# Optimization experiments

Measured on AMD Instinct MI355X. Metric: run time of the kernel, lower is better.

The kernel has to match this reference:

```python
import jax, jax.numpy as jnp
import numpy as np

N_DRUG = 572
EMB = 512
K_NB = 64
SEG_NB = 16
BN_EPS = 1e-5


def setup_inputs() -> dict:
    key = jax.random.key(0)
    ks = jax.random.split(key, 8)
    return {
        "drug_name": jnp.arange(N_DRUG, dtype=jnp.int64) if jax.config.jax_enable_x64 else jnp.arange(N_DRUG, dtype=jnp.int32),
        "adj_tail": jax.random.randint(ks[0], (N_DRUG, K_NB), 0, 100000),
        "adj_relation": jax.random.randint(ks[1], (N_DRUG, K_NB), 0, 200),
        "inv_adj_idx": jax.random.randint(ks[2], (N_DRUG, SEG_NB), 0, N_DRUG),
        "drug_table": jax.random.normal(ks[3], (N_DRUG, EMB), dtype=jnp.float32),
        "rela_table": jax.random.normal(ks[4], (200, EMB), dtype=jnp.float32),
        "ent_table": jax.random.normal(ks[5], (100000, EMB), dtype=jnp.float32),
        "W_lin": jax.random.normal(ks[6], (2 * EMB, EMB), dtype=jnp.float32) * (1.0 / np.sqrt(2 * EMB)),
        "b_lin": jnp.zeros((EMB,), jnp.float32),
        "bn_gamma": jnp.ones((EMB,), jnp.float32),
        "bn_beta": jnp.zeros((EMB,), jnp.float32),
        "epoch": 2,
    }


def _forward(drug_name, adj_tail, adj_relation, inv_adj_idx,
             drug_table, rela_table, ent_table, W_lin, b_lin,
             bn_gamma, bn_beta, epoch):
    # Embedding gathers
    drug_emb = drug_table[drug_name]          # [N, D]
    rel_emb = rela_table[adj_relation]        # [N, K, D]
    ent_emb = ent_table[adj_tail]             # [N, K, D]

    # KGCN-style attention over sampled neighbors: score_k = softmax(drug . rel_k)
    scores = jax.nn.softmax(jnp.einsum('nd,nkd->nk', drug_emb, rel_emb), axis=1)
    attended = jnp.einsum('nk,nkd->nd', scores, ent_emb)  # [N, D]

    # Linear -> ReLU -> BatchNorm1d (training-mode batch stats, biased var)
    e = jnp.concatenate([attended, drug_emb], axis=1)     # [N, 2D]
    h = jax.nn.relu(e @ W_lin + b_lin)                    # [N, D]
    mu = jnp.mean(h, axis=0)
    var = jnp.mean(jnp.square(h - mu), axis=0)
    drug_f = bn_gamma * (h - mu) * jax.lax.rsqrt(var + BN_EPS) + bn_beta

    if epoch > 1:
        # Sequential in-place neighbor averaging (faithful to the Python loop:
        # later drugs see already-updated rows).
        def body(f, x):
            i, pos = x
            avg = jnp.mean(f[pos], axis=0)                # [D]
            f = f.at[i].set((avg + f[i]) * 0.5)
            return f, None
        idxs = jnp.arange(N_DRUG)
        drug_f, _ = jax.lax.scan(body, drug_f, (idxs, inv_adj_idx))
    return drug_f


def reference(drug_name, adj_tail, adj_relation, inv_adj_idx,
              drug_table, rela_table, ent_table, W_lin, b_lin,
              bn_gamma, bn_beta, epoch):
    return _forward(drug_name, adj_tail, adj_relation, inv_adj_idx,
                    drug_table, rela_table, ent_table, W_lin, b_lin,
                    bn_gamma, bn_beta, epoch)
```

## Files before the change

### kernel.cpp

```cpp
#include <hip/hip_runtime.h>
#include <hip/hip_bf16.h>

#define N_DRUG 572
#define EMB    512
#define K_NB   64
#define SEG_NB 16
#define SCOLS  16

typedef __hip_bfloat16  bf16;
typedef __hip_bfloat162 bf162;

__device__ __forceinline__ float b2f(bf16 x){ return __bfloat162float(x); }
__device__ __forceinline__ float bflo(unsigned u){ return __uint_as_float(u << 16); }
__device__ __forceinline__ float bfhi(unsigned u){ return __uint_as_float(u & 0xffff0000u); }
__device__ __forceinline__ unsigned pack_bf2(float a, float b) {
    bf162 v; v.x = __float2bfloat16(a); v.y = __float2bfloat16(b);
    unsigned u; __builtin_memcpy(&u, &v, 4); return u;
}

template<typename T> __device__ __forceinline__ float ldf(const T* p);
template<> __device__ __forceinline__ float ldf<float>(const float* p){ return *p; }
template<> __device__ __forceinline__ float ldf<bf16>(const bf16* p){ return b2f(*p); }

template<typename T> __device__ __forceinline__ float2 ld2(const T* p);
template<> __device__ __forceinline__ float2 ld2<float>(const float* p){ return *(const float2*)p; }
template<> __device__ __forceinline__ float2 ld2<bf16>(const bf16* p){
    bf162 v = *(const bf162*)p; return make_float2(b2f(v.x), b2f(v.y));
}

template<typename T> __device__ __forceinline__ void st2(T* p, float x, float y);
template<> __device__ __forceinline__ void st2<float>(float* p, float x, float y){ *(float2*)p = make_float2(x, y); }
template<> __device__ __forceinline__ void st2<bf16>(bf16* p, float x, float y){
    bf162 v; v.x = __float2bfloat16(x); v.y = __float2bfloat16(y); *(bf162*)p = v;
}

struct F8 { float v[8]; };
template<typename T> __device__ __forceinline__ F8 ld8(const T* p);
template<> __device__ __forceinline__ F8 ld8<float>(const float* p){
    F8 r; const float4 a = ((const float4*)p)[0], b = ((const float4*)p)[1];
    r.v[0]=a.x; r.v[1]=a.y; r.v[2]=a.z; r.v[3]=a.w;
    r.v[4]=b.x; r.v[5]=b.y; r.v[6]=b.z; r.v[7]=b.w; return r;
}
template<> __device__ __forceinline__ F8 ld8<bf16>(const bf16* p){
    F8 r; const uint4 u = *(const uint4*)p;
    r.v[0]=bflo(u.x); r.v[1]=bfhi(u.x); r.v[2]=bflo(u.y); r.v[3]=bfhi(u.y);
    r.v[4]=bflo(u.z); r.v[5]=bfhi(u.z); r.v[6]=bflo(u.w); r.v[7]=bfhi(u.w);
    return r;
}

__device__ __forceinline__ bool idx_is64(const void* drug_name) {
    return ((const int*)drug_name)[1] == 0;
}
__device__ __forceinline__ int ld_idx(const void* p, int i, bool is64) {
    return is64 ? (int)((const long long*)p)[i] : ((const int*)p)[i];
}

__device__ __forceinline__ bool detect_bf16(const void* tab) {
    const int lane = threadIdx.x & 63;
    int hit = 0;
    if (lane < 32) {
        const unsigned u = ((const unsigned*)tab)[lane * 997];
        const unsigned e = (u >> 7) & 0xffu;
        hit = (e >= 110u && e <= 141u) ? 1 : 0;
    }
    return __popcll(__ballot(hit)) >= 24;
}

struct __align__(16) FwdSmem {
    float e[2 * EMB];
    float part[4][EMB];
    float sc[K_NB];
    int   tl[K_NB];
    int   rl[K_NB];
};

template<typename T>
__device__ void fwd_impl(FwdSmem& sm,
    const void* drug_name, const void* adj_tail, const void* adj_rel,
    const T* __restrict__ drug_table, const T* __restrict__ rela_table,
    const T* __restrict__ ent_table,  const T* __restrict__ W,
    const T* __restrict__ bl, T* __restrict__ h)
{
    const int  t    = threadIdx.x;
    const int  wave = t >> 6, lane = t & 63;
    const int  n    = blockIdx.x;
    const bool is64 = idx_is64(drug_name);

    {
        const int row = ld_idx(drug_name, n, is64);
        const float2 v = ld2(drug_table + (size_t)row * EMB + 2 * t);
        sm.e[EMB + 2 * t]     = v.x;
        sm.e[EMB + 2 * t + 1] = v.y;
        if (t < K_NB) {
            sm.tl[t] = ld_idx(adj_tail, n * K_NB + t, is64);
            sm.rl[t] = ld_idx(adj_rel,  n * K_NB + t, is64);
        }
    }
    __syncthreads();

    F8 ed;
    {
        const float4 e0 = ((const float4*)&sm.e[EMB + 8 * lane])[0];
        const float4 e1 = ((const float4*)&sm.e[EMB + 8 * lane])[1];
        ed.v[0]=e0.x; ed.v[1]=e0.y; ed.v[2]=e0.z; ed.v[3]=e0.w;
        ed.v[4]=e1.x; ed.v[5]=e1.y; ed.v[6]=e1.z; ed.v[7]=e1.w;
    }

    {
        #pragma unroll 4
        for (int kk = 0; kk < 16; ++kk) {
            const int k = 16 * wave + kk;
            const F8 rv = ld8(rela_table + (size_t)sm.rl[k] * EMB + 8 * lane);
            float p = 0.f;
            #pragma unroll
            for (int m = 0; m < 8; ++m) p = fmaf(ed.v[m], rv.v[m], p);
            #pragma unroll
            for (int off = 32; off; off >>= 1) p += __shfl_xor(p, off, 64);
            if (lane == 0) sm.sc[k] = p;
        }
    }
    __syncthreads();

    if (t < 64) {
        const float s = sm.sc[t];
        float m = s;
        #pragma unroll
        for (int off = 32; off; off >>= 1) m = fmaxf(m, __shfl_xor(m, off, 64));
        const float ex = __expf(s - m);
        float sum = ex;
        #pragma unroll
        for (int off = 32; off; off >>= 1) sum += __shfl_xor(sum, off, 64);
        sm.sc[t] = ex / sum;
    }
    __syncthreads();

    {
        float a[8];
        #pragma unroll
        for (int m = 0; m < 8; ++m) a[m] = 0.f;
        #pragma unroll 4
        for (int kk = 0; kk < 16; ++kk) {
            const int k = 16 * wave + kk;
            const float wgt = sm.sc[k];
            const F8 v = ld8(ent_table + (size_t)sm.tl[k] * EMB + 8 * lane);
            #pragma unroll
            for (int m = 0; m < 8; ++m) a[m] = fmaf(wgt, v.v[m], a[m]);
        }
        float4* pp = (float4*)&sm.part[wave][8 * lane];
        pp[0] = make_float4(a[0], a[1], a[2], a[3]);
        pp[1] = make_float4(a[4], a[5], a[6], a[7]);
    }
    __syncthreads();

    {
        float2 s = make_float2(0.f, 0.f);
        #pragma unroll
        for (int w = 0; w < 4; ++w) {
            const float2 pw = *(const float2*)&sm.part[w][2 * t];
            s.x += pw.x; s.y += pw.y;
        }
        sm.e[2 * t]     = s.x;
        sm.e[2 * t + 1] = s.y;
    }
    __syncthreads();

    {
        float acc[8];
        #pragma unroll
        for (int m = 0; m < 8; ++m) acc[m] = 0.f;
        const int j0 = wave * 256;
        #pragma unroll 4
        for (int j = 0; j < 256; ++j) {
            const float ej = sm.e[j0 + j];
            const F8 w8 = ld8(W + (size_t)(j0 + j) * EMB + 8 * lane);
            #pragma unroll
            for (int m = 0; m < 8; ++m) acc[m] = fmaf(ej, w8.v[m], acc[m]);
        }
        float4* pp = (float4*)&sm.part[wave][8 * lane];
        pp[0] = make_float4(acc[0], acc[1], acc[2], acc[3]);
        pp[1] = make_float4(acc[4], acc[5], acc[6], acc[7]);
    }
    __syncthreads();

    {
        const int d0 = 2 * t;
        const float2 bb = ld2(bl + d0);
        float x = bb.x, y = bb.y;
        #pragma unroll
        for (int w = 0; w < 4; ++w) {
            const float2 pw = *(const float2*)&sm.part[w][d0];
            x += pw.x; y += pw.y;
        }
        st2(h + (size_t)n * EMB + d0, fmaxf(x, 0.f), fmaxf(y, 0.f));
    }
}

__global__ __launch_bounds__(256) void k_fwd(
    const void* drug_name, const void* adj_tail, const void* adj_rel,
    const void* drug_tab, const void* rela_tab, const void* ent_tab,
    const void* W, const void* bl, void* h)
{
    __shared__ FwdSmem sm;
    if (detect_bf16(drug_tab))
        fwd_impl<bf16>(sm, drug_name, adj_tail, adj_rel,
                       (const bf16*)drug_tab, (const bf16*)rela_tab,
                       (const bf16*)ent_tab, (const bf16*)W,
                       (const bf16*)bl, (bf16*)h);
    else
        fwd_impl<float>(sm, drug_name, adj_tail, adj_rel,
                        (const float*)drug_tab, (const float*)rela_tab,
                        (const float*)ent_tab, (const float*)W,
                        (const float*)bl, (float*)h);
}

struct __align__(16) ScanSmem {
    float    fbuf[N_DRUG * SCOLS];
    unsigned obuf[N_DRUG * SEG_NB];
    float4   corr[576];
};

template<typename T>
__device__ __forceinline__ void stage_fbuf(float* fbuf, const T* h, int c0, int t);
template<>
__device__ __forceinline__ void stage_fbuf<float>(float* fbuf, const float* h, int c0, int t) {
    float4* dst = (float4*)fbuf;
    #pragma unroll 4
    for (int k = t; k < N_DRUG * 4; k += 64)
        dst[k] = *(const float4*)(h + (size_t)(k >> 2) * EMB + c0 + 4 * (k & 3));
}
template<>
__device__ __forceinline__ void stage_fbuf<bf16>(float* fbuf, const bf16* h, int c0, int t) {
    float4* dst = (float4*)fbuf;
    #pragma unroll 4
    for (int k = t; k < N_DRUG * 2; k += 64) {
        const uint4 v = *(const uint4*)(h + (size_t)(k >> 1) * EMB + c0 + 8 * (k & 1));
        dst[2 * k]     = make_float4(bflo(v.x), bfhi(v.x), bflo(v.y), bfhi(v.y));
        dst[2 * k + 1] = make_float4(bflo(v.z), bfhi(v.z), bflo(v.w), bfhi(v.w));
    }
}

template<typename T>
__device__ __forceinline__ void flush_fbuf(const float* fbuf, T* h, int c0, int t);
template<>
__device__ __forceinline__ void flush_fbuf<float>(const float* fbuf, float* h, int c0, int t) {
    const float4* src = (const float4*)fbuf;
    #pragma unroll 4
    for (int k = t; k < N_DRUG * 4; k += 64)
        *(float4*)(h + (size_t)(k >> 2) * EMB + c0 + 4 * (k & 3)) = src[k];
}
template<>
__device__ __forceinline__ void flush_fbuf<bf16>(const float* fbuf, bf16* h, int c0, int t) {
    const float4* src = (const float4*)fbuf;
    #pragma unroll 4
    for (int k = t; k < N_DRUG * 2; k += 64) {
        const float4 f0 = src[2 * k], f1 = src[2 * k + 1];
        uint4 o;
        o.x = pack_bf2(f0.x, f0.y); o.y = pack_bf2(f0.z, f0.w);
        o.z = pack_bf2(f1.x, f1.y); o.w = pack_bf2(f1.z, f1.w);
        *(uint4*)(h + (size_t)(k >> 1) * EMB + c0 + 8 * (k & 1)) = o;
    }
}

template<bool IS64>
__device__ __forceinline__ void stage_obuf(unsigned* obuf, const void* inv, int t) {
    const uint4* src = (const uint4*)inv;
    if (IS64) {
        #pragma unroll 4
        for (int k = t; k < (N_DRUG * SEG_NB) / 2; k += 64) {
            const uint4 v = src[k];
            *(uint2*)(obuf + 2 * k) = make_uint2(v.x << 4, v.z << 4);
        }
    } else {
        uint4* dst = (uint4*)obuf;
        #pragma unroll 4
        for (int k = t; k < (N_DRUG * SEG_NB) / 4; k += 64) {
            uint4 v = src[k];
            v.x <<= 4; v.y <<= 4; v.z <<= 4; v.w <<= 4;
            dst[k] = v;
        }
    }
}

#define RMIN(X) (((X) < N_DRUG) ? (X) : (N_DRUG - 1))

#define BODY4(Vg, Qg, Sc, Fc, Cc, Vr, Sr, I)                                 \
    {                                                                        \
        Vg.x = fb[Qg.x + c]; Vg.y = fb[Qg.y + c];                            \
        Vg.z = fb[Qg.z + c]; Vg.w = fb[Qg.w + c];                            \
        Qg = ob4[RMIN((I) + 7) * 4 + g];                                     \
        float nv = fmaf(Sc, 1.f / 32.f, Fc * 0.5f);                          \
        nv = fmaf(Cc.x, nv1 - f1, nv);                                       \
        nv = fmaf(Cc.y, nv2 - f2, nv);                                       \
        nv = fmaf(Cc.z, nv3 - f3, nv);                                       \
        f3 = f2; f2 = f1; f1 = Fc; nv3 = nv2; nv2 = nv1; nv1 = nv;           \
        if (g == 0) sm.fbuf[(I) * SCOLS + c] = nv;                           \
        Fc = fb[RMIN((I) + 4) * 16 + c];                                     \
        Cc = sm.corr[(I) + 4];                                               \
        float l = (Vr.x + Vr.y) + (Vr.z + Vr.w);                             \
        Sr = (l + __shfl_xor(l, 16, 64)) +                                   \
             (__shfl_xor(l, 32, 64) + __shfl_xor(l, 48, 64));                \
    }

template<typename T, bool IS64>
__device__ void scan_impl(ScanSmem& sm, T* __restrict__ h,
    const void* __restrict__ inv, const T* __restrict__ gamma,
    const T* __restrict__ beta, const void* __restrict__ epoch)
{
    const int t  = threadIdx.x;
    const int c0 = blockIdx.x * SCOLS;

    stage_obuf<IS64>(sm.obuf, inv, t);
    stage_fbuf<T>(sm.fbuf, h, c0, t);
    for (int k = t; k < 576; k += 64) sm.corr[k] = make_float4(0.f, 0.f, 0.f, 0.f);
    __syncthreads();

    for (int i = 1 + t; i < N_DRUG; i += 64) {
        const unsigned tA = (unsigned)(i - 1) << 4;
        const unsigned tB = (unsigned)(i - 2) << 4;
        const unsigned tC = (unsigned)(i - 3) << 4;
        int cA = 0, cB = 0, cC = 0;
        #pragma unroll
        for (int j = 0; j < SEG_NB; ++j) {
            const unsigned o = sm.obuf[i * SEG_NB + j];
            cA += (o == tA) ? 1 : 0;
            cB += (o == tB) ? 1 : 0;
            cC += (o == tC) ? 1 : 0;
        }
        sm.corr[i] = make_float4((float)cA * (1.f / 32.f),
                                 (float)cB * (1.f / 32.f),
                                 (float)cC * (1.f / 32.f), 0.f);
    }

    {
        const int c = t & 15, g = t >> 4;
        float s = 0.f, s2 = 0.f;
        for (int r = g; r < N_DRUG; r += 4) {
            const float x = sm.fbuf[r * SCOLS + c];
            s += x; s2 = fmaf(x, x, s2);
        }
        s  += __shfl_xor(s, 16, 64);  s  += __shfl_xor(s, 32, 64);
        s2 += __shfl_xor(s2, 16, 64); s2 += __shfl_xor(s2, 32, 64);
        const float mu  = s * (1.f / N_DRUG);
        const float var = fmaxf(s2 * (1.f / N_DRUG) - mu * mu, 0.f);
        const float gs  = ldf(gamma + c0 + c) * rsqrtf(var + 1e-5f);
        const float bs  = ldf(beta  + c0 + c);
        for (int r = g; r < N_DRUG; r += 4) {
            const float x = sm.fbuf[r * SCOLS + c];
            sm.fbuf[r * SCOLS + c] = fmaf(x - mu, gs, bs);
        }
    }
    __syncthreads();

    if (((const int*)epoch)[0] > 1) {
        const int c = t & 15, g = t >> 4;
        const float* fb  = sm.fbuf;
        const uint4* ob4 = (const uint4*)sm.obuf;

        float4 V0, V1, V2, V3;
        uint4  Q0, Q1, Q2, Q3;

        {
            const uint4 o0 = ob4[0 * 4 + g], o1 = ob4[1 * 4 + g], o2 = ob4[2 * 4 + g];
            V0.x = fb[o0.x + c]; V0.y = fb[o0.y + c];
            V0.z = fb[o0.z + c]; V0.w = fb[o0.w + c];
            V1.x = fb[o1.x + c]; V1.y = fb[o1.y + c];
            V1.z = fb[o1.z + c]; V1.w = fb[o1.w + c];
            V2.x = fb[o2.x + c]; V2.y = fb[o2.y + c];
            V2.z = fb[o2.z + c]; V2.w = fb[o2.w + c];
        }
        Q3 = ob4[3 * 4 + g];
        Q0 = ob4[4 * 4 + g]; Q1 = ob4[5 * 4 + g]; Q2 = ob4[6 * 4 + g];
        float F0 = fb[0 * 16 + c], F1 = fb[1 * 16 + c];
        float F2 = fb[2 * 16 + c], F3 = fb[3 * 16 + c];
        float4 C0 = sm.corr[0], C1 = sm.corr[1];
        float4 C2 = sm.corr[2], C3 = sm.corr[3];
        float S0, S1, S2 = 0.f, S3 = 0.f;
        {
            float l0 = (V0.x + V0.y) + (V0.z + V0.w);
            S0 = (l0 + __shfl_xor(l0, 16, 64)) +
                 (__shfl_xor(l0, 32, 64) + __shfl_xor(l0, 48, 64));
            float l1 = (V1.x + V1.y) + (V1.z + V1.w);
            S1 = (l1 + __shfl_xor(l1, 16, 64)) +
                 (__shfl_xor(l1, 32, 64) + __shfl_xor(l1, 48, 64));
        }
        float nv1 = 0.f, nv2 = 0.f, nv3 = 0.f, f1 = 0.f, f2 = 0.f, f3 = 0.f;

        for (int i = 0; i < N_DRUG; i += 4) {
            BODY4(V3, Q3, S0, F0, C0, V2, S2, i);
            BODY4(V0, Q0, S1, F1, C1, V3, S3, i + 1);
            BODY4(V1, Q1, S2, F2, C2, V0, S0, i + 2);
            BODY4(V2, Q2, S3, F3, C3, V1, S1, i + 3);
        }
    }
    __syncthreads();

    flush_fbuf<T>(sm.fbuf, h, c0, t);
}

__global__ __launch_bounds__(64) void k_scan(
    void* h, const void* inv, const void* gamma, const void* beta,
    const void* epoch, const void* drug_name, const void* drug_tab)
{
    __shared__ ScanSmem sm;
    const bool isbf = detect_bf16(drug_tab);
    const bool is64 = idx_is64(drug_name);
    if (isbf) {
        if (is64) scan_impl<bf16, true >(sm, (bf16*)h, inv, (const bf16*)gamma, (const bf16*)beta, epoch);
        else      scan_impl<bf16, false>(sm, (bf16*)h, inv, (const bf16*)gamma, (const bf16*)beta, epoch);
    } else {
        if (is64) scan_impl<float, true >(sm, (float*)h, inv, (const float*)gamma, (const float*)beta, epoch);
        else      scan_impl<float, false>(sm, (float*)h, inv, (const float*)gamma, (const float*)beta, epoch);
    }
}

extern "C" void kernel_launch(void* const* d_in, const int* in_sizes, int n_in,
                              void* d_out, int out_size, void* d_ws, size_t ws_size,
                              hipStream_t stream)
{
    (void)in_sizes; (void)n_in; (void)out_size; (void)d_ws; (void)ws_size;

    k_fwd<<<N_DRUG, 256, 0, stream>>>(
        d_in[0], d_in[1], d_in[2],
        d_in[4], d_in[5], d_in[6],
        d_in[7], d_in[8],
        d_out);
    k_scan<<<EMB / SCOLS, 64, 0, stream>>>(
        d_out, d_in[3],
        d_in[9], d_in[10], d_in[11],
        d_in[0], d_in[4]);
}
```

Baseline: 418.0 us.

## Split attention and linear layer into separate kernels with tiled GEMM

Splits the fused per-drug forward kernel in two. The first writes attended+drug embeddings to workspace, and the second runs the linear layer as a tiled GEMM over blocks of 16 rows by 64 columns. Each W element loaded is reused across 16 rows instead of being read once per drug, which cuts the repeated global loads of the 2MB weight matrix. The cost is an extra launch and a workspace round trip, and the old fused path is kept as a fallback when no workspace is available.

```diff
diff --git a/kernel.cpp b/kernel.cpp
--- a/kernel.cpp
+++ b/kernel.cpp
@@ -6,6 +6,8 @@
 #define K_NB   64
 #define SEG_NB 16
 #define SCOLS  16
+#define LM     16
+#define LN     64
 
 typedef __hip_bfloat16  bf16;
 typedef __hip_bfloat162 bf162;
@@ -75,15 +77,13 @@
 };
 
 template<typename T>
-__device__ void fwd_impl(FwdSmem& sm,
+__device__ void att_phases(FwdSmem& sm,
     const void* drug_name, const void* adj_tail, const void* adj_rel,
     const T* __restrict__ drug_table, const T* __restrict__ rela_table,
-    const T* __restrict__ ent_table,  const T* __restrict__ W,
-    const T* __restrict__ bl, T* __restrict__ h)
+    const T* __restrict__ ent_table, int n)
 {
     const int  t    = threadIdx.x;
     const int  wave = t >> 6, lane = t & 63;
-    const int  n    = blockIdx.x;
     const bool is64 = idx_is64(drug_name);
 
     {
@@ -151,7 +151,122 @@
         pp[1] = make_float4(a[4], a[5], a[6], a[7]);
     }
     __syncthreads();
-
+}
+
+template<typename T>
+__device__ void att_impl(FwdSmem& sm,
+    const void* drug_name, const void* adj_tail, const void* adj_rel,
+    const T* __restrict__ drug_table, const T* __restrict__ rela_table,
+    const T* __restrict__ ent_table, float* __restrict__ ews)
+{
+    const int t = threadIdx.x;
+    const int n = blockIdx.x;
+    att_phases<T>(sm, drug_name, adj_tail, adj_rel,
+                  drug_table, rela_table, ent_table, n);
+    {
+        const int d0 = 2 * t;
+        float2 s = make_float2(0.f, 0.f);
+        #pragma unroll
+        for (int w = 0; w < 4; ++w) {
+            const float2 pw = *(const float2*)&sm.part[w][d0];
+            s.x += pw.x; s.y += pw.y;
+        }
+        float* row = ews + (size_t)n * (2 * EMB);
+        *(float2*)&row[d0]       = s;
+        *(float2*)&row[EMB + d0] = *(const float2*)&sm.e[EMB + d0];
+    }
+}
+
+__global__ __launch_bounds__(256) void k_att(
+    const void* drug_name, const void* adj_tail, const void* adj_rel,
+    const void* drug_tab, const void* rela_tab, const void* ent_tab,
+    float* ews)
+{
+    __shared__ FwdSmem sm;
+    if (detect_bf16(drug_tab))
+        att_impl<bf16>(sm, drug_name, adj_tail, adj_rel,
+                       (const bf16*)drug_tab, (const bf16*)rela_tab,
+                       (const bf16*)ent_tab, ews);
+    else
+        att_impl<float>(sm, drug_name, adj_tail, adj_rel,
+                        (const float*)drug_tab, (const float*)rela_tab,
+                        (const float*)ent_tab, ews);
+}
+
+template<typename T>
+__device__ void lin_impl(float (&elds)[LM][2 * EMB], const float* __restrict__ ews,
+    const T* __restrict__ W, const T* __restrict__ bl, T* __restrict__ h)
+{
+    const int t  = threadIdx.x;
+    const int mb = blockIdx.x >> 3;
+    const int nb = blockIdx.x & 7;
+    const int m0 = mb * LM, n0 = nb * LN;
+
+    for (int k = t; k < LM * 256; k += 256) {
+        const int r = k >> 8, q = k & 255;
+        const int row = m0 + r;
+        ((float4*)elds[r])[q] = (row < N_DRUG)
+            ? ((const float4*)(ews + (size_t)row * (2 * EMB)))[q]
+            : make_float4(0.f, 0.f, 0.f, 0.f);
+    }
+    __syncthreads();
+
+    const int col = n0 + 2 * (t & 31);
+    const int d0  = 2 * (t >> 5);
+    const float4* e0 = (const float4*)elds[d0];
+    const float4* e1 = (const float4*)elds[d0 + 1];
+    float a00 = 0.f, a01 = 0.f, a10 = 0.f, a11 = 0.f;
+
+    #pragma unroll 4
+    for (int k4 = 0; k4 < (2 * EMB) / 4; ++k4) {
+        const float4 x0 = e0[k4];
+        const float4 x1 = e1[k4];
+        const T* Wp = W + (size_t)(4 * k4) * EMB + col;
+        const float2 w0 = ld2(Wp);
+        const float2 w1 = ld2(Wp + EMB);
+        const float2 w2 = ld2(Wp + 2 * EMB);
+        const float2 w3 = ld2(Wp + 3 * EMB);
+        a00 = fmaf(x0.x, w0.x, a00); a01 = fmaf(x0.x, w0.y, a01);
+        a10 = fmaf(x1.x, w0.x, a10); a11 = fmaf(x1.x, w0.y, a11);
+        a00 = fmaf(x0.y, w1.x, a00); a01 = fmaf(x0.y, w1.y, a01);
+        a10 = fmaf(x1.y, w1.x, a10); a11 = fmaf(x1.y, w1.y, a11);
+        a00 = fmaf(x0.z, w2.x, a00); a01 = fmaf(x0.z, w2.y, a01);
+        a10 = fmaf(x1.z, w2.x, a10); a11 = fmaf(x1.z, w2.y, a11);
+        a00 = fmaf(x0.w, w3.x, a00); a01 = fmaf(x0.w, w3.y, a01);
+        a10 = fmaf(x1.w, w3.x, a10); a11 = fmaf(x1.w, w3.y, a11);
+    }
+
+    const float2 bb = ld2(bl + col);
+    const int r0 = m0 + d0, r1 = r0 + 1;
+    if (r0 < N_DRUG)
+        st2(h + (size_t)r0 * EMB + col, fmaxf(a00 + bb.x, 0.f), fmaxf(a01 + bb.y, 0.f));
+    if (r1 < N_DRUG)
+        st2(h + (size_t)r1 * EMB + col, fmaxf(a10 + bb.x, 0.f), fmaxf(a11 + bb.y, 0.f));
+}
+
+__global__ __launch_bounds__(256) void k_lin(
+    const float* ews, const void* W, const void* bl, void* h,
+    const void* drug_tab)
+{
+    __shared__ float elds[LM][2 * EMB];
+    if (detect_bf16(drug_tab))
+        lin_impl<bf16>(elds, ews, (const bf16*)W, (const bf16*)bl, (bf16*)h);
+    else
+        lin_impl<float>(elds, ews, (const float*)W, (const float*)bl, (float*)h);
+}
+
+template<typename T>
+__device__ void fwd_impl(FwdSmem& sm,
+    const void* drug_name, const void* adj_tail, const void* adj_rel,
+    const T* __restrict__ drug_table, const T* __restrict__ rela_table,
+    const T* __restrict__ ent_table,  const T* __restrict__ W,
+    const T* __restrict__ bl, T* __restrict__ h)
+{
+    const int t = threadIdx.x;
+    const int wave = t >> 6, lane = t & 63;
+    const int n = blockIdx.x;
+    att_phases<T>(sm, drug_name, adj_tail, adj_rel,
+                  drug_table, rela_table, ent_table, n);
     {
         float2 s = make_float2(0.f, 0.f);
         #pragma unroll
@@ -163,7 +278,6 @@
         sm.e[2 * t + 1] = s.y;
     }
     __syncthreads();
-
     {
         float acc[8];
         #pragma unroll
@@ -181,7 +295,6 @@
         pp[1] = make_float4(acc[4], acc[5], acc[6], acc[7]);
     }
     __syncthreads();
-
     {
         const int d0 = 2 * t;
         const float2 bb = ld2(bl + d0);
@@ -417,13 +530,23 @@
                               void* d_out, int out_size, void* d_ws, size_t ws_size,
                               hipStream_t stream)
 {
-    (void)in_sizes; (void)n_in; (void)out_size; (void)d_ws; (void)ws_size;
-
-    k_fwd<<<N_DRUG, 256, 0, stream>>>(
-        d_in[0], d_in[1], d_in[2],
-        d_in[4], d_in[5], d_in[6],
-        d_in[7], d_in[8],
-        d_out);
+    (void)in_sizes; (void)n_in; (void)out_size;
+
+    const size_t ews_bytes = (size_t)N_DRUG * 2 * EMB * sizeof(float);
+    if (d_ws != nullptr && ws_size >= ews_bytes) {
+        k_att<<<N_DRUG, 256, 0, stream>>>(
+            d_in[0], d_in[1], d_in[2],
+            d_in[4], d_in[5], d_in[6],
+            (float*)d_ws);
+        k_lin<<<((N_DRUG + LM - 1) / LM) * (EMB / LN), 256, 0, stream>>>(
+            (const float*)d_ws, d_in[7], d_in[8], d_out, d_in[4]);
+    } else {
+        k_fwd<<<N_DRUG, 256, 0, stream>>>(
+            d_in[0], d_in[1], d_in[2],
+            d_in[4], d_in[5], d_in[6],
+            d_in[7], d_in[8],
+            d_out);
+    }
     k_scan<<<EMB / SCOLS, 64, 0, stream>>>(
         d_out, d_in[3],
         d_in[9], d_in[10], d_in[11],
```

New measurement: 426.4 us. +2.0%, slower.
